# Kernel tuning notes

Hardware: AMD Instinct MI355X
Metric: run time of the kernel (lower is better)

## Reference

```python
import jax, jax.numpy as jnp
from jax import lax
import numpy as np

B, C, H, W = 16, 32, 256, 256
K = 3  # kernel size, padding=1 -> SAME


def setup_inputs() -> dict:
    key = jax.random.key(0)
    k1, k2, k3, k4, k5, k6 = jax.random.split(key, 6)
    x = jax.random.normal(k1, (B, C, H, W), dtype=jnp.float32)
    gate_values = jax.random.uniform(k2, (B, C), dtype=jnp.float32)
    # Stacked per-output-channel Conv2d experts == one [C, C, K, K] conv (OIHW)
    fan_in = C * K * K
    bound = 1.0 / np.sqrt(fan_in)
    w1 = jax.random.uniform(k3, (C, C, K, K), minval=-bound, maxval=bound, dtype=jnp.float32)
    b1 = jax.random.uniform(k4, (C,), minval=-bound, maxval=bound, dtype=jnp.float32)
    w2 = jax.random.uniform(k5, (C, C, K, K), minval=-bound, maxval=bound, dtype=jnp.float32)
    b2 = jax.random.uniform(k6, (C,), minval=-bound, maxval=bound, dtype=jnp.float32)
    return {"x": x, "gate_values": gate_values, "w1": w1, "b1": b1, "w2": w2, "b2": b2}


def _moe_conv(x, w, b, g):
    # x: [B,C,H,W], w: [C,C,K,K] (OIHW), b: [C], g: [B,C] effective gate
    y = lax.conv_general_dilated(
        x, w, window_strides=(1, 1), padding='SAME',
        dimension_numbers=('NCHW', 'OIHW', 'NCHW'))
    y = y + b[None, :, None, None]
    return y * g[:, :, None, None]


def reference(x, gate_values, w1, b1, w2, b2):
    # gate rows with value <= 0 are never written -> output stays zero;
    # selected rows are multiplied by the gate value (bias included).
    g = gate_values * (gate_values > 0).astype(gate_values.dtype)
    h = jax.nn.relu(_moe_conv(x, w1, b1, g))
    h = jax.nn.relu(_moe_conv(h, w2, b2, g))
    return h + x
```

## Files before the change

kernel.cpp:

```cpp
#include <hip/hip_runtime.h>

#define BB 16
#define CC 32
#define HH 256
#define WW 256

#define TWV 30
#define TH 8
#define NT 4
#define CIP 36

typedef short bf16x8 __attribute__((ext_vector_type(8)));
typedef float f32x16 __attribute__((ext_vector_type(16)));

struct alignas(8)  U2 { unsigned x, y; };
struct alignas(16) U4 { U2 lo, hi; };

__device__ __forceinline__ unsigned short f2bf(float f) {
    unsigned u = __float_as_uint(f);
    u += 0x7fffu + ((u >> 16) & 1u);
    return (unsigned short)(u >> 16);
}

__device__ __forceinline__ unsigned cvtpk(float lo, float hi) {
    unsigned r;
    asm("v_cvt_pk_bf16_f32 %0, %1, %2" : "=v"(r) : "v"(lo), "v"(hi));
    return r;
}

__global__ void wprep(const float* __restrict__ w1, const float* __restrict__ w2,
                      unsigned short* __restrict__ wq) {
    int idx = blockIdx.x * 256 + threadIdx.x;
    if (idx >= 18 * 2 * 32 * 8) return;
    int j    = idx & 7;
    int n    = (idx >> 3) & 31;
    int half = (idx >> 8) & 1;
    int st   = idx >> 9;
    int s = st & 1, pos = st >> 1;
    int ci = s * 16 + half * 8 + j;
    int src = (n * CC + ci) * 9 + pos;
    wq[idx]        = f2bf(w1[src]);
    wq[9216 + idx] = f2bf(w2[src]);
}

__global__ __launch_bounds__(256, 2)
void conv_fused(const float* __restrict__ x,
                const unsigned short* __restrict__ wq,
                const float* __restrict__ b1v,
                const float* __restrict__ b2v,
                const float* __restrict__ gate,
                float* __restrict__ out)
{
    __shared__ unsigned short xs[TH + 2][34][CIP];
    __shared__ unsigned short hs[2][TH][34][CIP];
    __shared__ float gs[CC], bs1[CC], bs2[CC];

    const int t     = threadIdx.x;
    const int b     = blockIdx.z;
    const int x0    = blockIdx.x * TWV;
    const int ybase = blockIdx.y * (TH * NT);

    if (t < CC) {
        float gv = gate[b * CC + t];
        gs[t]  = gv > 0.f ? gv : 0.f;
        bs1[t] = b1v[t];
        bs2[t] = b2v[t];
    }

    const int lane = t & 63;
    const int wv   = t >> 6;
    const int col  = lane & 31;
    const int half = lane >> 5;
    const int r0 = wv * 2, r1 = r0 + 1;

    bf16x8 wf1[18], wf2[18];
    const U4* wq1 = (const U4*)wq;
    const U4* wq2 = (const U4*)(wq + 9216);
    #pragma unroll
    for (int st = 0; st < 18; ++st) {
        wf1[st] = __builtin_bit_cast(bf16x8, wq1[(st * 2 + half) * 32 + col]);
        wf2[st] = __builtin_bit_cast(bf16x8, wq2[(st * 2 + half) * 32 + col]);
    }

    const int yA = t / 34,        xA = t - yA * 34;
    const int pB = 256 + t;
    const int yB = pB / 34,       xB = pB - yB * 34;
    const bool hasB = t < 84;
    const float* xb = x + (size_t)b * CC * HH * WW;

    auto stage = [&](int rowT) {
        float va[32], vb[32];
        #pragma unroll
        for (int j = 0; j < 32; ++j) { va[j] = 0.f; vb[j] = 0.f; }
        const int gyA = rowT + yA, gxA = x0 - 2 + xA;
        if (gyA >= 0 && gyA < HH && gxA >= 0 && gxA < WW) {
            const float* pa = xb + (gyA * WW + gxA);
            #pragma unroll
            for (int j = 0; j < 32; ++j) va[j] = pa[j * (HH * WW)];
        }
        const int gyB = rowT + yB, gxB = x0 - 2 + xB;
        if (hasB && gyB >= 0 && gyB < HH && gxB >= 0 && gxB < WW) {
            const float* pb = xb + (gyB * WW + gxB);
            #pragma unroll
            for (int j = 0; j < 32; ++j) vb[j] = pb[j * (HH * WW)];
        }
        #pragma unroll
        for (int k = 0; k < 8; ++k) {
            U2 w; w.x = cvtpk(va[4 * k + 0], va[4 * k + 1]);
                  w.y = cvtpk(va[4 * k + 2], va[4 * k + 3]);
            *(U2*)&xs[yA][xA][4 * k] = w;
        }
        if (hasB) {
            #pragma unroll
            for (int k = 0; k < 8; ++k) {
                U2 w; w.x = cvtpk(vb[4 * k + 0], vb[4 * k + 1]);
                      w.y = cvtpk(vb[4 * k + 2], vb[4 * k + 3]);
                *(U2*)&xs[yB][xB][4 * k] = w;
            }
        }
    };

    auto conv1_iter = [&](int i) {
        f32x16 acc0 = {0,0,0,0,0,0,0,0,0,0,0,0,0,0,0,0};
        f32x16 acc1 = {0,0,0,0,0,0,0,0,0,0,0,0,0,0,0,0};
        const unsigned short* xsb0 = &xs[r0][col][half * 8];
        const unsigned short* xsb1 = &xs[r1][col][half * 8];
        #pragma unroll
        for (int st = 0; st < 18; ++st) {
            const int pos = st >> 1, s = st & 1;
            const int kh = pos / 3, kw = pos - kh * 3;
            const int off = (kh * 34 + kw) * CIP + s * 16;
            U4 xa, xv;
            xa.lo = *(const U2*)(xsb0 + off);
            xa.hi = *(const U2*)(xsb0 + off + 4);
            xv.lo = *(const U2*)(xsb1 + off);
            xv.hi = *(const U2*)(xsb1 + off + 4);
            acc0 = __builtin_amdgcn_mfma_f32_32x32x16_bf16(wf1[st], __builtin_bit_cast(bf16x8, xa), acc0, 0, 0, 0);
            acc1 = __builtin_amdgcn_mfma_f32_32x32x16_bf16(wf1[st], __builtin_bit_cast(bf16x8, xv), acc1, 0, 0, 0);
        }
        const int rowbase = ybase - 1 + 8 * i;
        const int gR0 = rowbase + r0, gR1 = rowbase + r1;
        const int gC  = x0 - 1 + col;
        const bool okC = (unsigned)gC < (unsigned)WW;
        const bool ok0 = okC && ((unsigned)gR0 < (unsigned)HH);
        const bool ok1 = okC && ((unsigned)gR1 < (unsigned)HH);
        unsigned short* h0 = &hs[i & 1][r0][col][0];
        unsigned short* h1 = &hs[i & 1][r1][col][0];
        #pragma unroll
        for (int g = 0; g < 4; ++g) {
            int c0 = 8 * g + 4 * half;
            float a0 = fmaxf((acc0[4 * g + 0] + bs1[c0 + 0]) * gs[c0 + 0], 0.f);
            float a1 = fmaxf((acc0[4 * g + 1] + bs1[c0 + 1]) * gs[c0 + 1], 0.f);
            float a2 = fmaxf((acc0[4 * g + 2] + bs1[c0 + 2]) * gs[c0 + 2], 0.f);
            float a3 = fmaxf((acc0[4 * g + 3] + bs1[c0 + 3]) * gs[c0 + 3], 0.f);
            if (!ok0) { a0 = 0.f; a1 = 0.f; a2 = 0.f; a3 = 0.f; }
            U2 w0; w0.x = cvtpk(a0, a1); w0.y = cvtpk(a2, a3);
            *(U2*)(h0 + c0) = w0;
            float d0 = fmaxf((acc1[4 * g + 0] + bs1[c0 + 0]) * gs[c0 + 0], 0.f);
            float d1 = fmaxf((acc1[4 * g + 1] + bs1[c0 + 1]) * gs[c0 + 1], 0.f);
            float d2 = fmaxf((acc1[4 * g + 2] + bs1[c0 + 2]) * gs[c0 + 2], 0.f);
            float d3 = fmaxf((acc1[4 * g + 3] + bs1[c0 + 3]) * gs[c0 + 3], 0.f);
            if (!ok1) { d0 = 0.f; d1 = 0.f; d2 = 0.f; d3 = 0.f; }
            U2 w1; w1.x = cvtpk(d0, d1); w1.y = cvtpk(d2, d3);
            *(U2*)(h1 + c0) = w1;
        }
    };

    auto conv2_iter = [&](int j) {
        f32x16 acc0 = {0,0,0,0,0,0,0,0,0,0,0,0,0,0,0,0};
        f32x16 acc1 = {0,0,0,0,0,0,0,0,0,0,0,0,0,0,0,0};
        const unsigned short* hb0 = &hs[j & 1][0][0][0];
        const unsigned short* hb1 = &hs[(j + 1) & 1][0][0][0];
        if (wv < 3) {
            const unsigned short* p0 = hb0 + (r0 * 34 + col) * CIP + half * 8;
            const unsigned short* p1 = hb0 + (r1 * 34 + col) * CIP + half * 8;
            #pragma unroll
            for (int st = 0; st < 18; ++st) {
                const int pos = st >> 1, s = st & 1;
                const int kh = pos / 3, kw = pos - kh * 3;
                const int off = (kh * 34 + kw) * CIP + s * 16;
                U4 xa, xv;
                xa.lo = *(const U2*)(p0 + off);
                xa.hi = *(const U2*)(p0 + off + 4);
                xv.lo = *(const U2*)(p1 + off);
                xv.hi = *(const U2*)(p1 + off + 4);
                acc0 = __builtin_amdgcn_mfma_f32_32x32x16_bf16(wf2[st], __builtin_bit_cast(bf16x8, xa), acc0, 0, 0, 0);
                acc1 = __builtin_amdgcn_mfma_f32_32x32x16_bf16(wf2[st], __builtin_bit_cast(bf16x8, xv), acc1, 0, 0, 0);
            }
        } else {
            const unsigned short* c0p = hb0 + col * CIP + half * 8;
            const unsigned short* c1p = hb1 + col * CIP + half * 8;
            #pragma unroll
            for (int st = 0; st < 18; ++st) {
                const int pos = st >> 1, s = st & 1;
                const int kh = pos / 3, kw = pos - kh * 3;
                const int q0 = 6 + kh, q1 = 7 + kh;
                const unsigned short* p0 = (q0 >= 8 ? c1p : c0p) + ((q0 & 7) * 34 + kw) * CIP + s * 16;
                const unsigned short* p1 = (q1 >= 8 ? c1p : c0p) + ((q1 & 7) * 34 + kw) * CIP + s * 16;
                U4 xa, xv;
                xa.lo = *(const U2*)(p0);
                xa.hi = *(const U2*)(p0 + 4);
                xv.lo = *(const U2*)(p1);
                xv.hi = *(const U2*)(p1 + 4);
                acc0 = __builtin_amdgcn_mfma_f32_32x32x16_bf16(wf2[st], __builtin_bit_cast(bf16x8, xa), acc0, 0, 0, 0);
                acc1 = __builtin_amdgcn_mfma_f32_32x32x16_bf16(wf2[st], __builtin_bit_cast(bf16x8, xv), acc1, 0, 0, 0);
            }
        }
        const int gO0 = ybase + 8 * j + r0;
        const int gO1 = gO0 + 1;
        const int gX  = x0 + col;
        const bool okN = (col < TWV) && (gX < WW);
        float* ob = out + (size_t)b * CC * HH * WW;
        const float* rb = x + (size_t)b * CC * HH * WW;
        if (okN) {
            #pragma unroll
            for (int reg = 0; reg < 16; ++reg) {
                int co = (reg & 3) + 8 * (reg >> 2) + 4 * half;
                int i0 = (co * HH + gO0) * WW + gX;
                int i1 = (co * HH + gO1) * WW + gX;
                float v0 = (acc0[reg] + bs2[co]) * gs[co];
                float v1 = (acc1[reg] + bs2[co]) * gs[co];
                ob[i0] = fmaxf(v0, 0.f) + rb[i0];
                ob[i1] = fmaxf(v1, 0.f) + rb[i1];
            }
        }
    };

    stage(ybase - 2);
    __syncthreads();
    conv1_iter(0);
    #pragma unroll 1
    for (int i = 1; i <= NT; ++i) {
        __syncthreads();
        stage(ybase - 2 + 8 * i);
        __syncthreads();
        conv1_iter(i);
        __syncthreads();
        conv2_iter(i - 1);
    }
}

extern "C" void kernel_launch(void* const* d_in, const int* in_sizes, int n_in,
                              void* d_out, int out_size, void* d_ws, size_t ws_size,
                              hipStream_t stream) {
    const float* x  = (const float*)d_in[0];
    const float* gv = (const float*)d_in[1];
    const float* w1 = (const float*)d_in[2];
    const float* b1 = (const float*)d_in[3];
    const float* w2 = (const float*)d_in[4];
    const float* b2 = (const float*)d_in[5];
    float* out = (float*)d_out;

    unsigned short* wq = (unsigned short*)d_ws;

    wprep<<<36, 256, 0, stream>>>(w1, w2, wq);

    dim3 grid((WW + TWV - 1) / TWV, HH / (TH * NT), BB);
    conv_fused<<<grid, 256, 0, stream>>>(x, wq, b1, b2, gv, out);
}
```

Before: 398.0 us.

## Pre-convert input to bf16 NHWC and prefetch next stage tile into registers

Adds a pre-pass kernel that converts x from fp32 NCHW into a bf16 NHWC workspace, so the fused conv stages each pixel with four 16-byte loads instead of 32 strided fp32 loads plus conversion. The staging is split into a load into registers and a later write to LDS, and the next tile's load is issued before the current conv1 compute to overlap global latency. The cost is an extra full pass over x (read fp32, write bf16), more workspace, and higher register pressure from holding the prefetched tile.

```diff
diff --git a/kernel.cpp b/kernel.cpp
--- a/kernel.cpp
+++ b/kernel.cpp
@@ -43,8 +43,33 @@
     wq[9216 + idx] = f2bf(w2[src]);
 }
 
+__global__ __launch_bounds__(256)
+void to_nhwc(const float* __restrict__ x, unsigned short* __restrict__ xbf) {
+    int id = blockIdx.x * 256 + threadIdx.x;
+    int b  = id >> 16;
+    int p  = id & 65535;
+    const float* xp = x + (size_t)b * CC * HH * WW + p;
+    U4 o[4];
+    #pragma unroll
+    for (int q = 0; q < 4; ++q) {
+        float v0 = xp[(q * 8 + 0) * (HH * WW)];
+        float v1 = xp[(q * 8 + 1) * (HH * WW)];
+        float v2 = xp[(q * 8 + 2) * (HH * WW)];
+        float v3 = xp[(q * 8 + 3) * (HH * WW)];
+        float v4 = xp[(q * 8 + 4) * (HH * WW)];
+        float v5 = xp[(q * 8 + 5) * (HH * WW)];
+        float v6 = xp[(q * 8 + 6) * (HH * WW)];
+        float v7 = xp[(q * 8 + 7) * (HH * WW)];
+        o[q].lo.x = cvtpk(v0, v1); o[q].lo.y = cvtpk(v2, v3);
+        o[q].hi.x = cvtpk(v4, v5); o[q].hi.y = cvtpk(v6, v7);
+    }
+    U4* dst = (U4*)(xbf + ((size_t)b * HH * WW + p) * CC);
+    dst[0] = o[0]; dst[1] = o[1]; dst[2] = o[2]; dst[3] = o[3];
+}
+
 __global__ __launch_bounds__(256, 2)
-void conv_fused(const float* __restrict__ x,
+void conv_fused(const unsigned short* __restrict__ xbf,
+                const float* __restrict__ x,
                 const unsigned short* __restrict__ wq,
                 const float* __restrict__ b1v,
                 const float* __restrict__ b2v,
@@ -86,37 +111,34 @@
     const int pB = 256 + t;
     const int yB = pB / 34,       xB = pB - yB * 34;
     const bool hasB = t < 84;
-    const float* xb = x + (size_t)b * CC * HH * WW;
-
-    auto stage = [&](int rowT) {
-        float va[32], vb[32];
-        #pragma unroll
-        for (int j = 0; j < 32; ++j) { va[j] = 0.f; vb[j] = 0.f; }
+    const unsigned short* xbfb = xbf + (size_t)b * HH * WW * CC;
+
+    U4 sa0, sa1, sa2, sa3, sb0, sb1, sb2, sb3;
+
+    auto stage_load = [&](int rowT) {
+        sa0.lo = {0u,0u}; sa0.hi = {0u,0u}; sa1 = sa0; sa2 = sa0; sa3 = sa0;
+        sb0 = sa0; sb1 = sa0; sb2 = sa0; sb3 = sa0;
         const int gyA = rowT + yA, gxA = x0 - 2 + xA;
         if (gyA >= 0 && gyA < HH && gxA >= 0 && gxA < WW) {
-            const float* pa = xb + (gyA * WW + gxA);
-            #pragma unroll
-            for (int j = 0; j < 32; ++j) va[j] = pa[j * (HH * WW)];
+            const U4* p = (const U4*)(xbfb + (size_t)(gyA * WW + gxA) * CC);
+            sa0 = p[0]; sa1 = p[1]; sa2 = p[2]; sa3 = p[3];
         }
         const int gyB = rowT + yB, gxB = x0 - 2 + xB;
         if (hasB && gyB >= 0 && gyB < HH && gxB >= 0 && gxB < WW) {
-            const float* pb = xb + (gyB * WW + gxB);
-            #pragma unroll
-            for (int j = 0; j < 32; ++j) vb[j] = pb[j * (HH * WW)];
-        }
-        #pragma unroll
-        for (int k = 0; k < 8; ++k) {
-            U2 w; w.x = cvtpk(va[4 * k + 0], va[4 * k + 1]);
-                  w.y = cvtpk(va[4 * k + 2], va[4 * k + 3]);
-            *(U2*)&xs[yA][xA][4 * k] = w;
-        }
+            const U4* p = (const U4*)(xbfb + (size_t)(gyB * WW + gxB) * CC);
+            sb0 = p[0]; sb1 = p[1]; sb2 = p[2]; sb3 = p[3];
+        }
+    };
+    auto stage_write = [&]() {
+        *(U2*)&xs[yA][xA][0]  = sa0.lo; *(U2*)&xs[yA][xA][4]  = sa0.hi;
+        *(U2*)&xs[yA][xA][8]  = sa1.lo; *(U2*)&xs[yA][xA][12] = sa1.hi;
+        *(U2*)&xs[yA][xA][16] = sa2.lo; *(U2*)&xs[yA][xA][20] = sa2.hi;
+        *(U2*)&xs[yA][xA][24] = sa3.lo; *(U2*)&xs[yA][xA][28] = sa3.hi;
         if (hasB) {
-            #pragma unroll
-            for (int k = 0; k < 8; ++k) {
-                U2 w; w.x = cvtpk(vb[4 * k + 0], vb[4 * k + 1]);
-                      w.y = cvtpk(vb[4 * k + 2], vb[4 * k + 3]);
-                *(U2*)&xs[yB][xB][4 * k] = w;
-            }
+            *(U2*)&xs[yB][xB][0]  = sb0.lo; *(U2*)&xs[yB][xB][4]  = sb0.hi;
+            *(U2*)&xs[yB][xB][8]  = sb1.lo; *(U2*)&xs[yB][xB][12] = sb1.hi;
+            *(U2*)&xs[yB][xB][16] = sb2.lo; *(U2*)&xs[yB][xB][20] = sb2.hi;
+            *(U2*)&xs[yB][xB][24] = sb3.lo; *(U2*)&xs[yB][xB][28] = sb3.hi;
         }
     };
 
@@ -226,14 +248,17 @@
         }
     };
 
-    stage(ybase - 2);
+    stage_load(ybase - 2);
+    stage_write();
     __syncthreads();
+    stage_load(ybase - 2 + 8);
     conv1_iter(0);
     #pragma unroll 1
     for (int i = 1; i <= NT; ++i) {
         __syncthreads();
-        stage(ybase - 2 + 8 * i);
+        stage_write();
         __syncthreads();
+        if (i < NT) stage_load(ybase - 2 + 8 * (i + 1));
         conv1_iter(i);
         __syncthreads();
         conv2_iter(i - 1);
@@ -251,10 +276,12 @@
     const float* b2 = (const float*)d_in[5];
     float* out = (float*)d_out;
 
-    unsigned short* wq = (unsigned short*)d_ws;
+    unsigned short* xbf = (unsigned short*)d_ws;
+    unsigned short* wq  = xbf + (size_t)BB * HH * WW * CC;
 
     wprep<<<36, 256, 0, stream>>>(w1, w2, wq);
+    to_nhwc<<<BB * HH * WW / 256, 256, 0, stream>>>(x, xbf);
 
     dim3 grid((WW + TWV - 1) / TWV, HH / (TH * NT), BB);
-    conv_fused<<<grid, 256, 0, stream>>>(x, wq, b1, b2, gv, out);
-}
+    conv_fused<<<grid, 256, 0, stream>>>(xbf, x, wq, b1, b2, gv, out);
+}
```

After: 465.0 us. +16.8%, slower.
